# Kernel optimization log

Measured on AMD Instinct MI355X. Metric: run time of the kernel, lower is better.

## Reference

```python
import jax, jax.numpy as jnp
import numpy as np

HEADS = 16
DIM_HEAD = 64
NPATCH = 256
LN_EPS = 1e-5


def setup_inputs() -> dict:
    key = jax.random.key(0)
    ks = jax.random.split(key, 6)
    B, S, D = 4, 2048, 1024
    inner = HEADS * DIM_HEAD  # 1024
    x = jax.random.normal(ks[0], (B, S, D), dtype=jnp.float32)
    ln_gamma = jnp.ones((D,), dtype=jnp.float32)
    ln_beta = jnp.zeros((D,), dtype=jnp.float32)
    # torch Linear: y = x @ W.T; we store the transposed weight directly.
    Wqkv = jax.random.normal(ks[1], (D, 3 * inner), dtype=jnp.float32) / np.sqrt(D)
    Wout = jax.random.normal(ks[2], (inner, D), dtype=jnp.float32) / np.sqrt(inner)
    bout = jnp.zeros((D,), dtype=jnp.float32)
    return {"x": x, "ln_gamma": ln_gamma, "ln_beta": ln_beta,
            "Wqkv": Wqkv, "Wout": Wout, "bout": bout}


def reference(x, ln_gamma, ln_beta, Wqkv, Wout, bout):
    B, S, D = x.shape
    # LayerNorm
    mu = jnp.mean(x, axis=-1, keepdims=True)
    var = jnp.mean(jnp.square(x - mu), axis=-1, keepdims=True)
    xn = (x - mu) * jax.lax.rsqrt(var + LN_EPS) * ln_gamma + ln_beta
    # QKV projection
    qkv = xn @ Wqkv  # [B, S, 3*H*Dh]
    q, k, v = jnp.split(qkv, 3, axis=-1)
    q = q.reshape(B, S, HEADS, DIM_HEAD)
    k = k.reshape(B, S, HEADS, DIM_HEAD)
    v = v.reshape(B, S, HEADS, DIM_HEAD)
    scale = DIM_HEAD ** -0.5
    dots = jnp.einsum('bqhd,bkhd->bhqk', q, k) * scale  # [B,H,S,S]
    # block-causal mask: query window i attends to key windows 0..i
    win = jnp.arange(S) // NPATCH
    mask = win[:, None] >= win[None, :]  # [S, S] bool
    dots = jnp.where(mask[None, None], dots, -jnp.inf)
    attn = jax.nn.softmax(dots, axis=-1)
    out = jnp.einsum('bhqk,bkhd->bqhd', attn, v).reshape(B, S, HEADS * DIM_HEAD)
    return out @ Wout + bout
```

## Files before the change

kernel.cpp:

```cpp
#include <hip/hip_runtime.h>
#include <stdint.h>

typedef unsigned short u16;
typedef __attribute__((ext_vector_type(8))) short bf16x8;
typedef __attribute__((ext_vector_type(4))) float f32x4;
typedef __attribute__((ext_vector_type(4))) unsigned short u16x4;
typedef __attribute__((ext_vector_type(4))) unsigned int u32x4;

#define DEVI static __device__ __forceinline__

#define QSCALE (0.125f * 1.4426950408889634f)

DEVI u16 f2bf(float f) {
  union { float f; unsigned int u; } v; v.f = f;
  unsigned int u = v.u + 0x7fffu + ((v.u >> 16) & 1u);
  return (u16)(u >> 16);
}
DEVI void gl16(const void* g, void* l) {
  __builtin_amdgcn_global_load_lds(
      (__attribute__((address_space(1))) void*)g,
      (__attribute__((address_space(3))) void*)l, 16, 0, 0);
}
DEVI unsigned int cvtpk(float a, float b) {
  unsigned int r;
  asm("v_cvt_pk_bf16_f32 %0, %1, %2" : "=v"(r) : "v"(a), "v"(b));
  return r;
}
DEVI float fexp2(float x) {
  float r;
  asm("v_exp_f32 %0, %1\n\ts_nop 0" : "=v"(r) : "v"(x));
  return r;
}
DEVI float fmax4(f32x4 v) {
  return fmaxf(fmaxf(v[0], v[1]), fmaxf(v[2], v[3]));
}

__global__ __launch_bounds__(256) void k_ln_split(
    const float* __restrict__ x, const float* __restrict__ gamma,
    const float* __restrict__ beta, u16* __restrict__ xh) {
  const int row = blockIdx.x;
  const int t = threadIdx.x;
  const float4* xr = (const float4*)(x + (size_t)row * 1024);
  float4 v = xr[t];
  float s = v.x + v.y + v.z + v.w;
  float s2 = v.x * v.x + v.y * v.y + v.z * v.z + v.w * v.w;
  #pragma unroll
  for (int m = 1; m < 64; m <<= 1) { s += __shfl_xor(s, m); s2 += __shfl_xor(s2, m); }
  __shared__ float ls[4], ls2[4];
  if ((t & 63) == 0) { ls[t >> 6] = s; ls2[t >> 6] = s2; }
  __syncthreads();
  s = ls[0] + ls[1] + ls[2] + ls[3];
  s2 = ls2[0] + ls2[1] + ls2[2] + ls2[3];
  float mu = s * (1.0f / 1024.0f);
  float var = s2 * (1.0f / 1024.0f) - mu * mu;
  float rstd = rsqrtf(var + 1e-5f);
  float4 g = ((const float4*)gamma)[t];
  float4 b = ((const float4*)beta)[t];
  float xv[4] = {v.x, v.y, v.z, v.w};
  float gg[4] = {g.x, g.y, g.z, g.w};
  float bb[4] = {b.x, b.y, b.z, b.w};
  u16x4 hv;
  #pragma unroll
  for (int i = 0; i < 4; i++) {
    float xn = (xv[i] - mu) * rstd * gg[i] + bb[i];
    hv[i] = f2bf(xn);
  }
  ((u16x4*)xh)[(size_t)row * 256 + t] = hv;
}

__global__ __launch_bounds__(256) void k_wsplit_t(
    const float* __restrict__ W, u16* __restrict__ Wth, int K, int N) {
  __shared__ float tile[32][33];
  const int t = threadIdx.x;
  const int tx = t & 31, ty = t >> 5;
  #pragma unroll
  for (int i = 0; i < 4; i++) {
    int k = blockIdx.y * 32 + ty + i * 8;
    int n = blockIdx.x * 32 + tx;
    tile[ty + i * 8][tx] = W[(size_t)k * N + n];
  }
  __syncthreads();
  #pragma unroll
  for (int i = 0; i < 4; i++) {
    int n = blockIdx.x * 32 + ty + i * 8;
    int k = blockIdx.y * 32 + tx;
    Wth[(size_t)n * K + k] = f2bf(tile[tx][ty + i * 8]);
  }
}

template <int MODE>
__global__ __launch_bounds__(256) void k_gemm(
    const u16* __restrict__ Ah, const u16* __restrict__ Bh,
    u16* __restrict__ Qh, u16* __restrict__ Kh, u16* __restrict__ Vth,
    float* __restrict__ Cout, const float* __restrict__ bias) {
  __shared__ u16 sAh[128 * 64];
  __shared__ u16 sBh[128 * 64];
  const int t = threadIdx.x, lane = t & 63, w = t >> 6;
  const int bm = blockIdx.x, bn = blockIdx.y;
  const int wm = (w >> 1) * 64, wn = (w & 1) * 64;
  const int g = lane >> 4, c = lane & 15;
  const size_t arow0 = (size_t)bm * 128, brow0 = (size_t)bn * 128;

  f32x4 acc[4][4] = {};

  for (int kt = 0; kt < 16; kt++) {
    __syncthreads();
    #pragma unroll
    for (int i = 0; i < 4; i++) {
      int ci = t + i * 256;
      int r = ci >> 3, cc = ci & 7;
      int cs = cc ^ (r & 7);
      size_t ka = (size_t)kt * 64 + cs * 8;
      gl16(Ah + (arow0 + r) * 1024 + ka, sAh + (size_t)ci * 8);
      gl16(Bh + (brow0 + r) * 1024 + ka, sBh + (size_t)ci * 8);
    }
    __syncthreads();
    #pragma unroll
    for (int ks = 0; ks < 2; ks++) {
      bf16x8 afh[4], bfh[4];
      #pragma unroll
      for (int mi = 0; mi < 4; mi++) {
        int row = wm + mi * 16 + c;
        afh[mi] = *(const bf16x8*)(sAh + row * 64 + (((ks * 4 + g) ^ (row & 7)) * 8));
      }
      #pragma unroll
      for (int ni = 0; ni < 4; ni++) {
        int row = wn + ni * 16 + c;
        bfh[ni] = *(const bf16x8*)(sBh + row * 64 + (((ks * 4 + g) ^ (row & 7)) * 8));
      }
      #pragma unroll
      for (int mi = 0; mi < 4; mi++)
        #pragma unroll
        for (int ni = 0; ni < 4; ni++)
          acc[mi][ni] = __builtin_amdgcn_mfma_f32_16x16x32_bf16(afh[mi], bfh[ni], acc[mi][ni], 0, 0, 0);
    }
  }

  if (MODE == 0) {
    #pragma unroll
    for (int mi = 0; mi < 4; mi++) {
      int grow0 = bm * 128 + wm + mi * 16 + g * 4;
      int b = grow0 >> 11, s0 = grow0 & 2047;
      #pragma unroll
      for (int ni = 0; ni < 4; ni++) {
        int gcol = bn * 128 + wn + ni * 16 + c;
        int which = gcol >> 10, rem = gcol & 1023;
        int hh = rem >> 6, dd = rem & 63;
        if (which == 2) {
          u16x4 hv;
          #pragma unroll
          for (int r = 0; r < 4; r++) hv[r] = f2bf(acc[mi][ni][r]);
          size_t off = ((size_t)((b * 16 + hh) * 64 + dd)) * 2048 + s0;
          *(u16x4*)(Vth + off) = hv;
        } else {
          u16* dh = which ? Kh : Qh;
          float sc = which ? 1.0f : QSCALE;
          #pragma unroll
          for (int r = 0; r < 4; r++) {
            size_t off = ((size_t)(b * 16 + hh) * 2048 + (s0 + r)) * 64 + dd;
            dh[off] = f2bf(acc[mi][ni][r] * sc);
          }
        }
      }
    }
  } else {
    #pragma unroll
    for (int mi = 0; mi < 4; mi++) {
      int grow0 = bm * 128 + wm + mi * 16 + g * 4;
      #pragma unroll
      for (int ni = 0; ni < 4; ni++) {
        int gcol = bn * 128 + wn + ni * 16 + c;
        float bb = bias[gcol];
        #pragma unroll
        for (int r = 0; r < 4; r++)
          Cout[(size_t)(grow0 + r) * 1024 + gcol] = acc[mi][ni][r] + bb;
      }
    }
  }
}

__global__ __launch_bounds__(512, 4) void k_attn(
    const u16* __restrict__ Qh, const u16* __restrict__ Kh,
    const u16* __restrict__ Vth, u16* __restrict__ Oh) {
  __shared__ u16 lK[2][128 * 64], lV[2][64 * 128];
  const int t = threadIdx.x, lane = t & 63, w = t >> 6;
  const int bh = blockIdx.x;
  const int qt = 15 - blockIdx.y;
  const int b = bh >> 4, h = bh & 15;
  const int qrow0 = qt * 128;
  const int kvlen = (qt / 2 + 1) * 256;
  const int g = lane >> 4, c = lane & 15;

  bf16x8 qf[2];
  {
    const u16* qb = Qh + ((size_t)bh * 2048 + qrow0 + w * 16) * 64;
    #pragma unroll
    for (int ks = 0; ks < 2; ks++)
      qf[ks] = *(const bf16x8*)(qb + (size_t)c * 64 + ks * 32 + g * 8);
  }

  const u16* Kb = Kh + (size_t)bh * 2048 * 64;
  const u16* Vb = Vth + (size_t)bh * 64 * 2048;

  int kbase[2], vbase[4];
  #pragma unroll
  for (int ks = 0; ks < 2; ks++) kbase[ks] = c * 64 + (((ks * 4 + g) ^ (c & 7)) * 8);
  #pragma unroll
  for (int ks = 0; ks < 4; ks++) vbase[ks] = c * 128 + (((ks * 4 + g) ^ c) * 8);

  const int kr0 = t >> 3, kcs0 = (t & 7) ^ (kr0 & 7);
  const int vr0 = t >> 4, vcs0 = (t & 15) ^ (vr0 & 15);

  const bf16x8 vones = {(short)0x3F80, (short)0x3F80, (short)0x3F80, (short)0x3F80,
                        (short)0x3F80, (short)0x3F80, (short)0x3F80, (short)0x3F80};

  float mrun = 0.f;
  f32x4 lsum = {0.f, 0.f, 0.f, 0.f};
  f32x4 o[4] = {};

  const int ntiles = kvlen >> 7;

  gl16(Kb + (size_t)kr0 * 64 + kcs0 * 8, lK[0] + (size_t)t * 8);
  gl16(Kb + (size_t)(kr0 + 64) * 64 + kcs0 * 8, lK[0] + (size_t)(t + 512) * 8);
  gl16(Vb + (size_t)vr0 * 2048 + vcs0 * 8, lV[0] + (size_t)t * 8);
  gl16(Vb + (size_t)(vr0 + 32) * 2048 + vcs0 * 8, lV[0] + (size_t)(t + 512) * 8);
  __syncthreads();

  const u16* gK = Kb + (size_t)(128 + kr0) * 64 + kcs0 * 8;
  const u16* gV = Vb + (size_t)vr0 * 2048 + 128 + vcs0 * 8;

  for (int kt = 0; kt < ntiles; kt++) {
    const int cur = kt & 1, nxt = cur ^ 1;
    if (kt + 1 < ntiles) {
      gl16(gK, lK[nxt] + (size_t)t * 8);
      gl16(gK + 64 * 64, lK[nxt] + (size_t)(t + 512) * 8);
      gl16(gV, lV[nxt] + (size_t)t * 8);
      gl16(gV + 32 * 2048, lV[nxt] + (size_t)(t + 512) * 8);
      gK += 128 * 64;  gV += 128;
    }

    f32x4 s[8];
    #pragma unroll
    for (int ni = 0; ni < 8; ni++)
      s[ni] = (f32x4){-mrun, -mrun, -mrun, -mrun};
    __builtin_amdgcn_s_setprio(1);
    #pragma unroll
    for (int ni = 0; ni < 8; ni++)
      #pragma unroll
      for (int ks = 0; ks < 2; ks++) {
        bf16x8 kf = *(const bf16x8*)(lK[cur] + ni * 1024 + kbase[ks]);
        s[ni] = __builtin_amdgcn_mfma_f32_16x16x32_bf16(kf, qf[ks], s[ni], 0, 0, 0);
      }
    __builtin_amdgcn_s_setprio(0);

    float tl = fmaxf(fmaxf(fmaxf(fmax4(s[0]), fmax4(s[1])), fmaxf(fmax4(s[2]), fmax4(s[3]))),
                     fmaxf(fmaxf(fmax4(s[4]), fmax4(s[5])), fmaxf(fmax4(s[6]), fmax4(s[7]))));
    if (!__all(tl <= 8.0f)) {
      float tm = fmaxf(tl, __shfl_xor(tl, 16));
      tm = fmaxf(tm, __shfl_xor(tm, 32));
      float delta = fmaxf(tm, 0.0f);
      mrun += delta;
      float al = fexp2(-delta);
      #pragma unroll
      for (int ni = 0; ni < 8; ni++)
        #pragma unroll
        for (int r = 0; r < 4; r++) s[ni][r] -= delta;
      #pragma unroll
      for (int r = 0; r < 4; r++) {
        float ar = __shfl(al, g * 4 + r);
        lsum[r] *= ar;
        #pragma unroll
        for (int di = 0; di < 4; di++) o[di][r] *= ar;
      }
    }

    bf16x8 pa[4];
    #pragma unroll
    for (int ks = 0; ks < 4; ks++) {
      unsigned int e0 = cvtpk(fexp2(s[2 * ks][0]), fexp2(s[2 * ks][1]));
      unsigned int e1 = cvtpk(fexp2(s[2 * ks][2]), fexp2(s[2 * ks][3]));
      unsigned int f0 = cvtpk(fexp2(s[2 * ks + 1][0]), fexp2(s[2 * ks + 1][1]));
      unsigned int f1 = cvtpk(fexp2(s[2 * ks + 1][2]), fexp2(s[2 * ks + 1][3]));
      asm volatile("v_permlane32_swap_b32 %0, %1" : "+v"(e0), "+v"(f0));
      asm volatile("v_permlane16_swap_b32 %0, %1" : "+v"(e0), "+v"(f0));
      asm volatile("v_permlane32_swap_b32 %0, %1" : "+v"(e1), "+v"(f1));
      asm volatile("v_permlane16_swap_b32 %0, %1" : "+v"(e1), "+v"(f1));
      union { u32x4 u; bf16x8 bv; } cvu;
      cvu.u = (u32x4){e0, e1, f0, f1};
      pa[ks] = cvu.bv;
    }

    __builtin_amdgcn_s_setprio(1);
    #pragma unroll
    for (int di = 0; di < 4; di++)
      #pragma unroll
      for (int ks = 0; ks < 4; ks++) {
        bf16x8 vf = *(const bf16x8*)(lV[cur] + di * 2048 + vbase[ks]);
        o[di] = __builtin_amdgcn_mfma_f32_16x16x32_bf16(pa[ks], vf, o[di], 0, 0, 0);
      }
    #pragma unroll
    for (int ks = 0; ks < 4; ks++)
      lsum = __builtin_amdgcn_mfma_f32_16x16x32_bf16(pa[ks], vones, lsum, 0, 0, 0);
    __builtin_amdgcn_s_setprio(0);

    __syncthreads();
  }

  #pragma unroll
  for (int r = 0; r < 4; r++) {
    float ir = 1.0f / lsum[r];
    int srow = qrow0 + w * 16 + g * 4 + r;
    size_t rowo = ((size_t)b * 2048 + srow) * 1024 + h * 64;
    #pragma unroll
    for (int di = 0; di < 4; di++)
      Oh[rowo + di * 16 + c] = f2bf(o[di][r] * ir);
  }
}

extern "C" void kernel_launch(void* const* d_in, const int* in_sizes, int n_in,
                              void* d_out, int out_size, void* d_ws, size_t ws_size,
                              hipStream_t stream) {
  const float* x     = (const float*)d_in[0];
  const float* gamma = (const float*)d_in[1];
  const float* beta  = (const float*)d_in[2];
  const float* Wqkv  = (const float*)d_in[3];
  const float* Wout  = (const float*)d_in[4];
  const float* bout  = (const float*)d_in[5];
  float* out = (float*)d_out;

  char* ws = (char*)d_ws;
  size_t off = 0;
  auto alloc = [&](size_t bytes) { char* p = ws + off; off += (bytes + 255) & ~(size_t)255; return p; };
  const size_t SZ_XN = (size_t)8192 * 1024 * 2;
  const size_t SZ_WQ = (size_t)3072 * 1024 * 2;
  const size_t SZ_WO = (size_t)1024 * 1024 * 2;
  const size_t SZ_QKV = (size_t)4 * 16 * 2048 * 64 * 2;
  u16* xnh  = (u16*)alloc(SZ_XN);
  u16* wqth = (u16*)alloc(SZ_WQ);
  u16* woth = (u16*)alloc(SZ_WO);
  u16* Qh  = (u16*)alloc(SZ_QKV);
  u16* Kh  = (u16*)alloc(SZ_QKV);
  u16* Vth = (u16*)alloc(SZ_QKV);
  if (off > ws_size) return;

  k_ln_split<<<8192, 256, 0, stream>>>(x, gamma, beta, xnh);
  k_wsplit_t<<<dim3(96, 32), 256, 0, stream>>>(Wqkv, wqth, 1024, 3072);
  k_wsplit_t<<<dim3(32, 32), 256, 0, stream>>>(Wout, woth, 1024, 1024);
  k_gemm<0><<<dim3(64, 24), 256, 0, stream>>>(xnh, wqth,
                                              Qh, Kh, Vth, nullptr, nullptr);
  k_attn<<<dim3(64, 16), 512, 0, stream>>>(Qh, Kh, Vth, xnh);
  k_gemm<1><<<dim3(64, 8), 256, 0, stream>>>(xnh, woth,
                                             nullptr, nullptr, nullptr,
                                             out, bout);
}
```

Baseline: 163.9 us.

## Double-buffer LDS tiles in GEMM to overlap global loads with MFMA

Splits the GEMM's shared-memory A/B tiles into two buffers and prefetches the next k-tile with global_load_lds while MFMAs run on the current one. It also drops one of the two barriers per iteration and hoists address arithmetic into precomputed pointers. The aim is to hide global-to-LDS latency behind compute, at the cost of doubling LDS use (64 KB per block), which may reduce occupancy. Correctness relies on the single trailing barrier also covering completion of the async LDS loads.

```diff
diff --git a/kernel.cpp b/kernel.cpp
--- a/kernel.cpp
+++ b/kernel.cpp
@@ -93,40 +93,51 @@
     const u16* __restrict__ Ah, const u16* __restrict__ Bh,
     u16* __restrict__ Qh, u16* __restrict__ Kh, u16* __restrict__ Vth,
     float* __restrict__ Cout, const float* __restrict__ bias) {
-  __shared__ u16 sAh[128 * 64];
-  __shared__ u16 sBh[128 * 64];
+  __shared__ u16 sA[2][128 * 64];
+  __shared__ u16 sB[2][128 * 64];
   const int t = threadIdx.x, lane = t & 63, w = t >> 6;
   const int bm = blockIdx.x, bn = blockIdx.y;
   const int wm = (w >> 1) * 64, wn = (w & 1) * 64;
   const int g = lane >> 4, c = lane & 15;
   const size_t arow0 = (size_t)bm * 128, brow0 = (size_t)bn * 128;
 
+  const int r0 = t >> 3, cc0 = t & 7;
+  const int cs0 = cc0 ^ (r0 & 7);
+  const u16* gA = Ah + (arow0 + r0) * 1024 + cs0 * 8;
+  const u16* gB = Bh + (brow0 + r0) * 1024 + cs0 * 8;
+
   f32x4 acc[4][4] = {};
 
+  #pragma unroll
+  for (int i = 0; i < 4; i++) {
+    gl16(gA + (size_t)i * 32768, sA[0] + (size_t)(t + i * 256) * 8);
+    gl16(gB + (size_t)i * 32768, sB[0] + (size_t)(t + i * 256) * 8);
+  }
+  gA += 64; gB += 64;
+  __syncthreads();
+
   for (int kt = 0; kt < 16; kt++) {
-    __syncthreads();
-    #pragma unroll
-    for (int i = 0; i < 4; i++) {
-      int ci = t + i * 256;
-      int r = ci >> 3, cc = ci & 7;
-      int cs = cc ^ (r & 7);
-      size_t ka = (size_t)kt * 64 + cs * 8;
-      gl16(Ah + (arow0 + r) * 1024 + ka, sAh + (size_t)ci * 8);
-      gl16(Bh + (brow0 + r) * 1024 + ka, sBh + (size_t)ci * 8);
-    }
-    __syncthreads();
+    const int cur = kt & 1, nxt = cur ^ 1;
+    if (kt + 1 < 16) {
+      #pragma unroll
+      for (int i = 0; i < 4; i++) {
+        gl16(gA + (size_t)i * 32768, sA[nxt] + (size_t)(t + i * 256) * 8);
+        gl16(gB + (size_t)i * 32768, sB[nxt] + (size_t)(t + i * 256) * 8);
+      }
+      gA += 64; gB += 64;
+    }
     #pragma unroll
     for (int ks = 0; ks < 2; ks++) {
       bf16x8 afh[4], bfh[4];
       #pragma unroll
       for (int mi = 0; mi < 4; mi++) {
         int row = wm + mi * 16 + c;
-        afh[mi] = *(const bf16x8*)(sAh + row * 64 + (((ks * 4 + g) ^ (row & 7)) * 8));
+        afh[mi] = *(const bf16x8*)(sA[cur] + row * 64 + (((ks * 4 + g) ^ (row & 7)) * 8));
       }
       #pragma unroll
       for (int ni = 0; ni < 4; ni++) {
         int row = wn + ni * 16 + c;
-        bfh[ni] = *(const bf16x8*)(sBh + row * 64 + (((ks * 4 + g) ^ (row & 7)) * 8));
+        bfh[ni] = *(const bf16x8*)(sB[cur] + row * 64 + (((ks * 4 + g) ^ (row & 7)) * 8));
       }
       #pragma unroll
       for (int mi = 0; mi < 4; mi++)
@@ -134,6 +145,7 @@
         for (int ni = 0; ni < 4; ni++)
           acc[mi][ni] = __builtin_amdgcn_mfma_f32_16x16x32_bf16(afh[mi], bfh[ni], acc[mi][ni], 0, 0, 0);
     }
+    __syncthreads();
   }
 
   if (MODE == 0) {
```

After: 164.0 us. Within noise of the previous version (+0.0%).
